# Performance work log

Hardware: AMD Instinct MI355X
Metric: run time of the kernel (lower is better)

The kernel has to match this reference:

```python
import jax, jax.numpy as jnp
import numpy as np

B, S, D, H, L, MAXSEQ = 32, 512, 768, 1024, 4, 1024


def setup_inputs() -> dict:
    key = jax.random.key(0)
    ks = jax.random.split(key, 10)
    s_in = 1.0 / np.sqrt(H)
    inp = {
        "x": jax.random.normal(ks[0], (B, S, D), dtype=jnp.float32),
        "pos_emb": jax.random.normal(ks[1], (1, MAXSEQ, D), dtype=jnp.float32),
        # layer 0 input->hidden weights (GRU: 3 gates stacked)
        "W_ih0": jax.random.uniform(ks[2], (3 * H, D), jnp.float32, -s_in, s_in),
        # layers 1..L-1 input->hidden weights
        "W_ih": jax.random.uniform(ks[3], (L - 1, 3 * H, H), jnp.float32, -s_in, s_in),
        "W_hh": jax.random.uniform(ks[4], (L, 3 * H, H), jnp.float32, -s_in, s_in),
        "b_ih": jax.random.uniform(ks[5], (L, 3 * H), jnp.float32, -s_in, s_in),
        "b_hh": jax.random.uniform(ks[6], (L, 3 * H), jnp.float32, -s_in, s_in),
        "W_out": jax.random.uniform(ks[7], (D, H), jnp.float32, -s_in, s_in),
        "b_out": jax.random.uniform(ks[8], (D,), jnp.float32, -s_in, s_in),
    }
    return inp


def _gru_cell(x, h, Wih, Whh, bih, bhh):
    # torch.nn.GRUCell math; gates stacked [r, z, n]
    gi = x @ Wih.T + bih  # [B, 3H]
    gh = h @ Whh.T + bhh  # [B, 3H]
    i_r, i_z, i_n = jnp.split(gi, 3, axis=-1)
    h_r, h_z, h_n = jnp.split(gh, 3, axis=-1)
    r = jax.nn.sigmoid(i_r + h_r)
    z = jax.nn.sigmoid(i_z + h_z)
    n = jnp.tanh(i_n + r * h_n)
    return (1.0 - z) * n + z * h


def reference(x, pos_emb, W_ih0, W_ih, W_hh, b_ih, b_hh, W_out, b_out):
    b, s, _ = x.shape
    xp = x + pos_emb[:, :s, :]          # add positional embedding
    xs = jnp.swapaxes(xp, 0, 1)         # [S, B, D] for scan over time

    def step(hs, xt):                   # hs: [L, B, H]
        inp = xt
        new_hs = []
        for l in range(L):
            Wih = W_ih0 if l == 0 else W_ih[l - 1]
            h = _gru_cell(inp, hs[l], Wih, W_hh[l], b_ih[l], b_hh[l])
            new_hs.append(h)
            inp = h
        return jnp.stack(new_hs), inp

    h0 = jnp.zeros((L, b, H), dtype=x.dtype)
    hs_final, outs = jax.lax.scan(step, h0, xs)  # outs: [S, B, H]
    out_seq = jnp.swapaxes(outs, 0, 1) @ W_out.T + b_out  # [B, S, D]
    return out_seq, hs_final
```

## Files before the change

### kernel.cpp

```cpp
#include <hip/hip_runtime.h>

#define B_ 32
#define S_ 512
#define D_ 768
#define H_ 1024
#define L_ 4
#define TH 3072
#define NPL 64
#define NITER (S_ + L_ - 1)

typedef unsigned short u16;
typedef unsigned int u32;
typedef __bf16 bf16x8 __attribute__((ext_vector_type(8)));
typedef float f32x4 __attribute__((ext_vector_type(4)));

__device__ __forceinline__ u16 f2b(float f) {
  unsigned u = __builtin_bit_cast(unsigned, f);
  u += 0x7fffu + ((u >> 16) & 1u);
  return (u16)(u >> 16);
}
__device__ __forceinline__ float b2f(u16 h) {
  return __builtin_bit_cast(float, ((unsigned)h) << 16);
}
__device__ __forceinline__ unsigned pack2(float a, float b) {
  return (unsigned)f2b(a) | ((unsigned)f2b(b) << 16);
}

__global__ __launch_bounds__(256) void cvt_kernel(const float* __restrict__ src,
                                                  u16* __restrict__ dst, int n4) {
  int i = blockIdx.x * 256 + threadIdx.x;
  int stride = gridDim.x * 256;
  for (; i < n4; i += stride) {
    float4 f = ((const float4*)src)[i];
    uint2 o;
    o.x = pack2(f.x, f.y);
    o.y = pack2(f.z, f.w);
    ((uint2*)dst)[i] = o;
  }
}

__global__ __launch_bounds__(256) void gi0_gemm(const float* __restrict__ x,
                                                const float* __restrict__ pos,
                                                const u16* __restrict__ W0,
                                                const float* __restrict__ bih0,
                                                u16* __restrict__ GI0) {
  const int n0 = blockIdx.x * 64;
  const int m0 = blockIdx.y * 64;
  __shared__ u16 sA[64 * 72];
  __shared__ u16 sB[64 * 72];
  const int tid = threadIdx.x, lane = tid & 63, wid = tid >> 6;
  const int wm = wid >> 1, wn = wid & 1;
  const int fr = lane & 15, fk = (lane >> 4) * 8;
  f32x4 acc[2][2] = {};
  for (int k0 = 0; k0 < D_; k0 += 64) {
    for (int sl = tid; sl < 512; sl += 256) {
      int r = sl >> 3, c = sl & 7;
      int m = m0 + r, si = m >> 5, b = m & 31;
      const float* xp = x + (size_t)((b << 9) + si) * D_ + k0 + c * 8;
      const float* pp = pos + (size_t)si * D_ + k0 + c * 8;
      float4 x0 = *(const float4*)xp, x1 = *(const float4*)(xp + 4);
      float4 p0 = *(const float4*)pp, p1 = *(const float4*)(pp + 4);
      uint4 o;
      o.x = pack2(x0.x + p0.x, x0.y + p0.y);
      o.y = pack2(x0.z + p0.z, x0.w + p0.w);
      o.z = pack2(x1.x + p1.x, x1.y + p1.y);
      o.w = pack2(x1.z + p1.z, x1.w + p1.w);
      *(uint4*)&sA[r * 72 + c * 8] = o;
      *(uint4*)&sB[r * 72 + c * 8] =
          *(const uint4*)(W0 + (size_t)(n0 + r) * D_ + k0 + c * 8);
    }
    __syncthreads();
#pragma unroll
    for (int kk = 0; kk < 2; ++kk) {
      bf16x8 a0 = *(const bf16x8*)&sA[(wm * 32 + fr) * 72 + kk * 32 + fk];
      bf16x8 a1 = *(const bf16x8*)&sA[(wm * 32 + 16 + fr) * 72 + kk * 32 + fk];
      bf16x8 b0 = *(const bf16x8*)&sB[(wn * 32 + fr) * 72 + kk * 32 + fk];
      bf16x8 b1 = *(const bf16x8*)&sB[(wn * 32 + 16 + fr) * 72 + kk * 32 + fk];
      acc[0][0] = __builtin_amdgcn_mfma_f32_16x16x32_bf16(a0, b0, acc[0][0], 0, 0, 0);
      acc[0][1] = __builtin_amdgcn_mfma_f32_16x16x32_bf16(a0, b1, acc[0][1], 0, 0, 0);
      acc[1][0] = __builtin_amdgcn_mfma_f32_16x16x32_bf16(a1, b0, acc[1][0], 0, 0, 0);
      acc[1][1] = __builtin_amdgcn_mfma_f32_16x16x32_bf16(a1, b1, acc[1][1], 0, 0, 0);
    }
    __syncthreads();
  }
#pragma unroll
  for (int mi = 0; mi < 2; ++mi)
#pragma unroll
    for (int ni = 0; ni < 2; ++ni)
#pragma unroll
      for (int r = 0; r < 4; ++r) {
        int m = m0 + wm * 32 + mi * 16 + (lane >> 4) * 4 + r;
        int n = n0 + wn * 32 + ni * 16 + fr;
        GI0[(size_t)m * TH + n] = f2b(acc[mi][ni][r] + bih0[n]);
      }
}

__global__ __launch_bounds__(256) void out_gemm(const u16* __restrict__ H3,
                                                const u16* __restrict__ Wo,
                                                const float* __restrict__ bo,
                                                float* __restrict__ out) {
  const int n0 = blockIdx.x * 64;
  const int m0 = blockIdx.y * 64;
  __shared__ u16 sA[64 * 72];
  __shared__ u16 sB[64 * 72];
  const int tid = threadIdx.x, lane = tid & 63, wid = tid >> 6;
  const int wm = wid >> 1, wn = wid & 1;
  const int fr = lane & 15, fk = (lane >> 4) * 8;
  f32x4 acc[2][2] = {};
  for (int k0 = 0; k0 < H_; k0 += 64) {
    for (int sl = tid; sl < 512; sl += 256) {
      int r = sl >> 3, c = sl & 7;
      int m = m0 + r, b = m >> 9, si = m & 511;
      *(uint4*)&sA[r * 72 + c * 8] =
          *(const uint4*)(H3 + (size_t)((si << 5) + b) * H_ + k0 + c * 8);
      *(uint4*)&sB[r * 72 + c * 8] =
          *(const uint4*)(Wo + (size_t)(n0 + r) * H_ + k0 + c * 8);
    }
    __syncthreads();
#pragma unroll
    for (int kk = 0; kk < 2; ++kk) {
      bf16x8 a0 = *(const bf16x8*)&sA[(wm * 32 + fr) * 72 + kk * 32 + fk];
      bf16x8 a1 = *(const bf16x8*)&sA[(wm * 32 + 16 + fr) * 72 + kk * 32 + fk];
      bf16x8 b0 = *(const bf16x8*)&sB[(wn * 32 + fr) * 72 + kk * 32 + fk];
      bf16x8 b1 = *(const bf16x8*)&sB[(wn * 32 + 16 + fr) * 72 + kk * 32 + fk];
      acc[0][0] = __builtin_amdgcn_mfma_f32_16x16x32_bf16(a0, b0, acc[0][0], 0, 0, 0);
      acc[0][1] = __builtin_amdgcn_mfma_f32_16x16x32_bf16(a0, b1, acc[0][1], 0, 0, 0);
      acc[1][0] = __builtin_amdgcn_mfma_f32_16x16x32_bf16(a1, b0, acc[1][0], 0, 0, 0);
      acc[1][1] = __builtin_amdgcn_mfma_f32_16x16x32_bf16(a1, b1, acc[1][1], 0, 0, 0);
    }
    __syncthreads();
  }
#pragma unroll
  for (int mi = 0; mi < 2; ++mi)
#pragma unroll
    for (int ni = 0; ni < 2; ++ni)
#pragma unroll
      for (int r = 0; r < 4; ++r) {
        int m = m0 + wm * 32 + mi * 16 + (lane >> 4) * 4 + r;
        int n = n0 + wn * 32 + ni * 16 + fr;
        out[(size_t)m * D_ + n] = acc[mi][ni][r] + bo[n];
      }
}

__global__ __launch_bounds__(256, 1) void rnn_persist(
    const u16* __restrict__ Whh, const u16* __restrict__ Wih,
    const u16* __restrict__ GI0, const float* __restrict__ bih,
    const float* __restrict__ bhh, u16* __restrict__ hg ,
    int* flags , u16* __restrict__ H3, float* __restrict__ hsf) {
  const int bid = blockIdx.x;
  const int l = bid >> 6;
  const int n0 = (bid & 63) << 4;
  const int tid = threadIdx.x, lane = tid & 63, wid = tid >> 6;
  const int fr = lane & 15, q = lane >> 4;

  __shared__ float red[4][3][32][17];

  bf16x8 w[3][16];
  if (l == 0) {
    const int kb = wid << 8;
#pragma unroll
    for (int g = 0; g < 3; ++g)
#pragma unroll
      for (int kt = 0; kt < 8; ++kt)
        w[g][kt] = *(const bf16x8*)(Whh + (((size_t)((g << 10) + n0 + fr)) << 10) +
                                    kb + kt * 32 + q * 8);
  } else {
    const u16* Wp = (wid < 2) ? (Wih + (((size_t)(l - 1) * TH) << 10))
                              : (Whh + (((size_t)l * TH) << 10));
    const int kb = (wid & 1) << 9;
#pragma unroll
    for (int g = 0; g < 3; ++g)
#pragma unroll
      for (int kt = 0; kt < 16; ++kt)
        w[g][kt] = *(const bf16x8*)(Wp + (((size_t)((g << 10) + n0 + fr)) << 10) +
                                    kb + kt * 32 + q * 8);
  }

  const int* f_own = flags + ((l << 6) + lane) * 16;
  const int* f_m1 = (l > 0) ? flags + (((l - 1) << 6) + lane) * 16 : f_own;
  const int* f_p1 = (l < 3) ? flags + (((l + 1) << 6) + lane) * 16 : f_own;
  int* f_mine = flags + ((l << 6) + (bid & 63)) * 16;

  const int gb = tid >> 3;
  const int gjj = (tid & 7) * 2;
  const int gj = n0 + gjj;
  float bihv[3][2], bhhv[3][2];
#pragma unroll
  for (int g = 0; g < 3; ++g) {
    if (l > 0) {
      bihv[g][0] = bih[l * TH + (g << 10) + gj];
      bihv[g][1] = bih[l * TH + (g << 10) + gj + 1];
    } else {
      bihv[g][0] = bihv[g][1] = 0.f;
    }
    bhhv[g][0] = bhh[l * TH + (g << 10) + gj];
    bhhv[g][1] = bhh[l * TH + (g << 10) + gj + 1];
  }
  float hpriv0 = 0.f, hpriv1 = 0.f;
  __syncthreads();

  for (int s = 0; s < NITER; ++s) {
    const int t = s - l;
    if (t < 0 || t >= S_) {
      if (tid == 0) {
        int v = s + 1;
        asm volatile("global_store_dword %0, %1, off sc0 sc1" ::"v"(f_mine), "v"(v)
                     : "memory");
      }
      continue;
    }
    const int prev = (s - 1) & 3;

    u32 g0p = 0, g1p = 0, g2p = 0;
    if (l == 0) {
      const u16* gp = GI0 + (size_t)((t << 5) + gb) * TH + gj;
      g0p = *(const u32*)gp;
      g1p = *(const u32*)(gp + 1024);
      g2p = *(const u32*)(gp + 2048);
    }

    if (wid == 0) {
      for (;;) {
        int fo, fm, fp;
        asm volatile(
            "global_load_dword %0, %3, off sc0 sc1\n\t"
            "global_load_dword %1, %4, off sc0 sc1\n\t"
            "global_load_dword %2, %5, off sc0 sc1\n\t"
            "s_waitcnt vmcnt(0)"
            : "=&v"(fo), "=&v"(fm), "=&v"(fp)
            : "v"(f_own), "v"(f_m1), "v"(f_p1)
            : "memory");
        __builtin_amdgcn_sched_barrier(0);
        bool ok = (fo >= s) && (fm >= s) && (fp >= s - 2);
        if (__all(ok)) break;
        __builtin_amdgcn_s_sleep(1);
      }
    }
    __syncthreads();

    f32x4 acc[2][3] = {};
    if (l == 0) {
      const u16* hp = hg + ((0 | prev) << 15);
      const int kb = wid << 8;
      bf16x8 afr[2][8];
#pragma unroll
      for (int mt = 0; mt < 2; ++mt)
#pragma unroll
        for (int kt = 0; kt < 8; ++kt) {
          const u16* p = hp + (((mt << 4) + fr) << 10) + kb + kt * 32 + q * 8;
          asm volatile("global_load_dwordx4 %0, %1, off sc0 sc1"
                       : "=v"(afr[mt][kt]) : "v"(p) : "memory");
        }
      asm volatile("s_waitcnt vmcnt(0)" ::: "memory");
      __builtin_amdgcn_sched_barrier(0);
#pragma unroll
      for (int kt = 0; kt < 8; ++kt)
#pragma unroll
        for (int g = 0; g < 3; ++g) {
          acc[0][g] = __builtin_amdgcn_mfma_f32_16x16x32_bf16(afr[0][kt], w[g][kt], acc[0][g], 0, 0, 0);
          acc[1][g] = __builtin_amdgcn_mfma_f32_16x16x32_bf16(afr[1][kt], w[g][kt], acc[1][g], 0, 0, 0);
        }
    } else {
      const u16* hsrc = (wid < 2) ? (hg + ((((l - 1) << 2) | prev) << 15))
                                  : (hg + (((l << 2) | prev) << 15));
      const int kb = (wid & 1) << 9;
      bf16x8 afr[2][16];
#pragma unroll
      for (int mt = 0; mt < 2; ++mt)
#pragma unroll
        for (int kt = 0; kt < 16; ++kt) {
          const u16* p = hsrc + (((mt << 4) + fr) << 10) + kb + kt * 32 + q * 8;
          asm volatile("global_load_dwordx4 %0, %1, off sc0 sc1"
                       : "=v"(afr[mt][kt]) : "v"(p) : "memory");
        }
      asm volatile("s_waitcnt vmcnt(0)" ::: "memory");
      __builtin_amdgcn_sched_barrier(0);
#pragma unroll
      for (int kt = 0; kt < 16; ++kt)
#pragma unroll
        for (int g = 0; g < 3; ++g) {
          acc[0][g] = __builtin_amdgcn_mfma_f32_16x16x32_bf16(afr[0][kt], w[g][kt], acc[0][g], 0, 0, 0);
          acc[1][g] = __builtin_amdgcn_mfma_f32_16x16x32_bf16(afr[1][kt], w[g][kt], acc[1][g], 0, 0, 0);
        }
    }

#pragma unroll
    for (int mt = 0; mt < 2; ++mt)
#pragma unroll
      for (int g = 0; g < 3; ++g)
#pragma unroll
        for (int r = 0; r < 4; ++r)
          red[wid][g][(mt << 4) + q * 4 + r][fr] = acc[mt][g][r];
    __syncthreads();

    float gi[3][2], gh[3][2];
#pragma unroll
    for (int g = 0; g < 3; ++g)
#pragma unroll
      for (int u = 0; u < 2; ++u) {
        float s01 = red[0][g][gb][gjj + u] + red[1][g][gb][gjj + u];
        float s23 = red[2][g][gb][gjj + u] + red[3][g][gb][gjj + u];
        if (l == 0) {
          gh[g][u] = s01 + s23 + bhhv[g][u];
        } else {
          gi[g][u] = s01 + bihv[g][u];
          gh[g][u] = s23 + bhhv[g][u];
        }
      }
    if (l == 0) {
      gi[0][0] = b2f((u16)(g0p & 0xffff));
      gi[0][1] = b2f((u16)(g0p >> 16));
      gi[1][0] = b2f((u16)(g1p & 0xffff));
      gi[1][1] = b2f((u16)(g1p >> 16));
      gi[2][0] = b2f((u16)(g2p & 0xffff));
      gi[2][1] = b2f((u16)(g2p >> 16));
    }
    float hn[2];
    float hpv[2] = {hpriv0, hpriv1};
#pragma unroll
    for (int u = 0; u < 2; ++u) {
      float rr = 1.f / (1.f + __expf(-(gi[0][u] + gh[0][u])));
      float zz = 1.f / (1.f + __expf(-(gi[1][u] + gh[1][u])));
      float xn = gi[2][u] + rr * gh[2][u];
      float nn = 1.f - 2.f / (__expf(2.f * xn) + 1.f);
      hn[u] = (1.f - zz) * nn + zz * hpv[u];
    }
    hpriv0 = hn[0];
    hpriv1 = hn[1];
    u32 hpack = pack2(hn[0], hn[1]);
    u32* hd = (u32*)(hg + (((l << 2) | (s & 3)) << 15) + (gb << 10) + gj);
    asm volatile("global_store_dword %0, %1, off sc0 sc1" ::"v"(hd), "v"(hpack)
                 : "memory");
    asm volatile("s_waitcnt vmcnt(0)" ::: "memory");
    __syncthreads();
    if (tid == 0) {
      int v = s + 1;
      asm volatile("global_store_dword %0, %1, off sc0 sc1" ::"v"(f_mine), "v"(v)
                   : "memory");
    }
    if (l == 3) *(u32*)(H3 + (((size_t)(t << 5) + gb) << 10) + gj) = hpack;
    if (t == S_ - 1) {
      hsf[((l << 5) + gb) * 1024 + gj] = hn[0];
      hsf[((l << 5) + gb) * 1024 + gj + 1] = hn[1];
    }
  }
}

extern "C" void kernel_launch(void* const* d_in, const int* in_sizes, int n_in,
                              void* d_out, int out_size, void* d_ws, size_t ws_size,
                              hipStream_t stream) {
  const float* x = (const float*)d_in[0];
  const float* pos = (const float*)d_in[1];
  const float* Wih0 = (const float*)d_in[2];
  const float* Wih = (const float*)d_in[3];
  const float* Whh = (const float*)d_in[4];
  const float* bih = (const float*)d_in[5];
  const float* bhh = (const float*)d_in[6];
  const float* Wout = (const float*)d_in[7];
  const float* bout = (const float*)d_in[8];
  float* out = (float*)d_out;

  char* ws = (char*)d_ws;
  size_t o = 0;
  u16* wih0_b = (u16*)(ws + o); o += (size_t)TH * D_ * 2;
  u16* wih_b  = (u16*)(ws + o); o += (size_t)3 * TH * H_ * 2;
  u16* whh_b  = (u16*)(ws + o); o += (size_t)4 * TH * H_ * 2;
  u16* wout_b = (u16*)(ws + o); o += (size_t)D_ * H_ * 2;
  u16* GI0    = (u16*)(ws + o); o += (size_t)S_ * B_ * TH * 2;
  u16* H3     = (u16*)(ws + o); o += (size_t)S_ * B_ * H_ * 2;
  u16* hg     = (u16*)(ws + o); o += (size_t)L_ * 4 * B_ * H_ * 2;
  int* flags  = (int*)(ws + o); o += (size_t)L_ * 64 * 16 * 4;

  cvt_kernel<<<512, 256, 0, stream>>>(Wih0, wih0_b, TH * D_ / 4);
  cvt_kernel<<<512, 256, 0, stream>>>(Wih, wih_b, 3 * TH * H_ / 4);
  cvt_kernel<<<512, 256, 0, stream>>>(Whh, whh_b, 4 * TH * H_ / 4);
  cvt_kernel<<<512, 256, 0, stream>>>(Wout, wout_b, D_ * H_ / 4);
  hipMemsetAsync(hg, 0, (size_t)L_ * 4 * B_ * H_ * 2 + (size_t)L_ * 64 * 16 * 4, stream);

  gi0_gemm<<<dim3(TH / 64, (S_ * B_) / 64), 256, 0, stream>>>(x, pos, wih0_b, bih, GI0);

  float* hsf = out + (size_t)B_ * S_ * D_;
  rnn_persist<<<256, 256, 0, stream>>>(whh_b, wih_b, GI0, bih, bhh, hg, flags, H3, hsf);

  out_gemm<<<dim3(D_ / 64, (S_ * B_) / 64), 256, 0, stream>>>(H3, wout_b, bout, out);
}
```

Before: 3.809 ms.

## Use 128 larger persistent blocks staging hidden state in LDS via direct loads

The persistent GRU kernel now runs 128 blocks of 512 threads instead of 256 blocks of 256 threads, with each block owning 32 output columns. Each step copies the previous hidden state(s) into LDS once per block with global_load_lds, and the waves read their MFMA A fragments from LDS rather than each wave loading them from global memory. The point is to cut duplicated global traffic for the hidden state and the number of blocks the flag barrier has to synchronise. In exchange each block needs about 129 KB of dynamic LDS, adds extra __syncthreads per step, and reads the biases from global memory inside the loop.

```diff
diff --git a/kernel.cpp b/kernel.cpp
--- a/kernel.cpp
+++ b/kernel.cpp
@@ -6,8 +6,10 @@
 #define H_ 1024
 #define L_ 4
 #define TH 3072
-#define NPL 64
+#define NPL 32
 #define NITER (S_ + L_ - 1)
+#define LDS_BUF 66048
+#define LDS_TOTAL 132096
 
 typedef unsigned short u16;
 typedef unsigned int u32;
@@ -142,60 +144,52 @@
       }
 }
 
-__global__ __launch_bounds__(256, 1) void rnn_persist(
+__global__ __launch_bounds__(512, 2) void rnn_persist(
     const u16* __restrict__ Whh, const u16* __restrict__ Wih,
     const u16* __restrict__ GI0, const float* __restrict__ bih,
     const float* __restrict__ bhh, u16* __restrict__ hg ,
     int* flags , u16* __restrict__ H3, float* __restrict__ hsf) {
+  extern __shared__ char smem[];
   const int bid = blockIdx.x;
-  const int l = bid >> 6;
-  const int n0 = (bid & 63) << 4;
+  const int l = bid >> 5;
+  const int n0 = (bid & 31) << 5;
   const int tid = threadIdx.x, lane = tid & 63, wid = tid >> 6;
   const int fr = lane & 15, q = lane >> 4;
-
-  __shared__ float red[4][3][32][17];
+  const int l32 = lane & 31;
+  const int nh = wid & 1;
 
   bf16x8 w[3][16];
   if (l == 0) {
-    const int kb = wid << 8;
+    const int kb = (wid >> 1) << 8;
 #pragma unroll
     for (int g = 0; g < 3; ++g)
 #pragma unroll
       for (int kt = 0; kt < 8; ++kt)
-        w[g][kt] = *(const bf16x8*)(Whh + (((size_t)((g << 10) + n0 + fr)) << 10) +
-                                    kb + kt * 32 + q * 8);
+        w[g][kt] = *(const bf16x8*)(
+            Whh + (((size_t)((g << 10) + n0 + nh * 16 + fr)) << 10) + kb +
+            kt * 32 + q * 8);
   } else {
-    const u16* Wp = (wid < 2) ? (Wih + (((size_t)(l - 1) * TH) << 10))
-                              : (Whh + (((size_t)l * TH) << 10));
-    const int kb = (wid & 1) << 9;
+    const int mat = wid >> 2;
+    const u16* Wp = (mat == 0) ? (Wih + (((size_t)(l - 1) * TH) << 10))
+                               : (Whh + (((size_t)l * TH) << 10));
+    const int kb = ((wid >> 1) & 1) << 9;
 #pragma unroll
     for (int g = 0; g < 3; ++g)
 #pragma unroll
       for (int kt = 0; kt < 16; ++kt)
-        w[g][kt] = *(const bf16x8*)(Wp + (((size_t)((g << 10) + n0 + fr)) << 10) +
-                                    kb + kt * 32 + q * 8);
+        w[g][kt] = *(const bf16x8*)(
+            Wp + (((size_t)((g << 10) + n0 + nh * 16 + fr)) << 10) + kb +
+            kt * 32 + q * 8);
   }
 
-  const int* f_own = flags + ((l << 6) + lane) * 16;
-  const int* f_m1 = (l > 0) ? flags + (((l - 1) << 6) + lane) * 16 : f_own;
-  const int* f_p1 = (l < 3) ? flags + (((l + 1) << 6) + lane) * 16 : f_own;
-  int* f_mine = flags + ((l << 6) + (bid & 63)) * 16;
-
-  const int gb = tid >> 3;
-  const int gjj = (tid & 7) * 2;
-  const int gj = n0 + gjj;
-  float bihv[3][2], bhhv[3][2];
-#pragma unroll
-  for (int g = 0; g < 3; ++g) {
-    if (l > 0) {
-      bihv[g][0] = bih[l * TH + (g << 10) + gj];
-      bihv[g][1] = bih[l * TH + (g << 10) + gj + 1];
-    } else {
-      bihv[g][0] = bihv[g][1] = 0.f;
-    }
-    bhhv[g][0] = bhh[l * TH + (g << 10) + gj];
-    bhhv[g][1] = bhh[l * TH + (g << 10) + gj + 1];
-  }
+  const int* f_own = flags + ((l << 5) + l32) * 16;
+  const int* f_m1 = (l > 0) ? flags + (((l - 1) << 5) + l32) * 16 : f_own;
+  const int* f_p1 = (l < 3) ? flags + (((l + 1) << 5) + l32) * 16 : f_own;
+  int* f_mine = flags + ((l << 5) + (bid & 31)) * 16;
+
+  const int gb = tid >> 4;
+  const int jj = (tid & 15) * 2;
+  const int gj = n0 + jj;
   float hpriv0 = 0.f, hpriv1 = 0.f;
   __syncthreads();
 
@@ -238,75 +232,104 @@
     }
     __syncthreads();
 
+    {
+      const u16* srcA = (l == 0) ? (hg + (prev << 15))
+                                 : (hg + ((((l - 1) << 2) | prev) << 15));
+      if (l == 0) {
+#pragma unroll
+        for (int ii = 0; ii < 8; ++ii) {
+          int i = wid * 8 + ii;
+          int row = i >> 1, half = i & 1;
+          const u16* sp = srcA + (row << 10) + half * 512 + lane * 8;
+          char* dp = smem + row * 2064 + half * 1024;
+          __builtin_amdgcn_global_load_lds(
+              (const __attribute__((address_space(1))) void*)sp,
+              (__attribute__((address_space(3))) void*)dp, 16, 0, 17);
+        }
+      } else {
+        const u16* srcB = hg + (((l << 2) | prev) << 15);
+#pragma unroll
+        for (int ii = 0; ii < 16; ++ii) {
+          int i = wid * 16 + ii;
+          int buf = i >> 6, j = i & 63, row = j >> 1, half = j & 1;
+          const u16* sp =
+              (buf ? srcB : srcA) + (row << 10) + half * 512 + lane * 8;
+          char* dp = smem + buf * LDS_BUF + row * 2064 + half * 1024;
+          __builtin_amdgcn_global_load_lds(
+              (const __attribute__((address_space(1))) void*)sp,
+              (__attribute__((address_space(3))) void*)dp, 16, 0, 17);
+        }
+      }
+      asm volatile("s_waitcnt vmcnt(0)" ::: "memory");
+    }
+    __syncthreads();
+
     f32x4 acc[2][3] = {};
     if (l == 0) {
-      const u16* hp = hg + ((0 | prev) << 15);
-      const int kb = wid << 8;
-      bf16x8 afr[2][8];
+      const int kqb = (wid >> 1) << 9;
+      const char* base = smem;
+#pragma unroll
+      for (int kt = 0; kt < 8; ++kt) {
+        int colb = kqb + kt * 64 + q * 16;
+        bf16x8 a0 = *(const bf16x8*)(base + fr * 2064 + colb);
+        bf16x8 a1 = *(const bf16x8*)(base + (16 + fr) * 2064 + colb);
+#pragma unroll
+        for (int g = 0; g < 3; ++g) {
+          acc[0][g] = __builtin_amdgcn_mfma_f32_16x16x32_bf16(a0, w[g][kt], acc[0][g], 0, 0, 0);
+          acc[1][g] = __builtin_amdgcn_mfma_f32_16x16x32_bf16(a1, w[g][kt], acc[1][g], 0, 0, 0);
+        }
+      }
+    } else {
+      const int khb = (((wid >> 1) & 1)) << 10;
+      const char* base = smem + (wid >> 2) * LDS_BUF;
+#pragma unroll
+      for (int kt = 0; kt < 16; ++kt) {
+        int colb = khb + kt * 64 + q * 16;
+        bf16x8 a0 = *(const bf16x8*)(base + fr * 2064 + colb);
+        bf16x8 a1 = *(const bf16x8*)(base + (16 + fr) * 2064 + colb);
+#pragma unroll
+        for (int g = 0; g < 3; ++g) {
+          acc[0][g] = __builtin_amdgcn_mfma_f32_16x16x32_bf16(a0, w[g][kt], acc[0][g], 0, 0, 0);
+          acc[1][g] = __builtin_amdgcn_mfma_f32_16x16x32_bf16(a1, w[g][kt], acc[1][g], 0, 0, 0);
+        }
+      }
+    }
+    __syncthreads();
+
+    {
+      float* red = (float*)smem;
+      const int slot = wid >> 1;
 #pragma unroll
       for (int mt = 0; mt < 2; ++mt)
 #pragma unroll
-        for (int kt = 0; kt < 8; ++kt) {
-          const u16* p = hp + (((mt << 4) + fr) << 10) + kb + kt * 32 + q * 8;
-          asm volatile("global_load_dwordx4 %0, %1, off sc0 sc1"
-                       : "=v"(afr[mt][kt]) : "v"(p) : "memory");
+        for (int g = 0; g < 3; ++g)
+#pragma unroll
+          for (int r = 0; r < 4; ++r)
+            red[((slot * 3 + g) * 32 + mt * 16 + q * 4 + r) * 33 + nh * 16 + fr] =
+                acc[mt][g][r];
+    }
+    __syncthreads();
+
+    float gi[3][2], gh[3][2];
+    {
+      const float* red = (const float*)smem;
+#pragma unroll
+      for (int g = 0; g < 3; ++g)
+#pragma unroll
+        for (int u = 0; u < 2; ++u) {
+          float s0 = red[((0 + g) * 32 + gb) * 33 + jj + u];
+          float s1 = red[((3 + g) * 32 + gb) * 33 + jj + u];
+          float s2 = red[((6 + g) * 32 + gb) * 33 + jj + u];
+          float s3 = red[((9 + g) * 32 + gb) * 33 + jj + u];
+          float bh = bhh[l * TH + (g << 10) + gj + u];
+          if (l == 0) {
+            gh[g][u] = s0 + s1 + s2 + s3 + bh;
+          } else {
+            gi[g][u] = s0 + s1 + bih[l * TH + (g << 10) + gj + u];
+            gh[g][u] = s2 + s3 + bh;
+          }
         }
-      asm volatile("s_waitcnt vmcnt(0)" ::: "memory");
-      __builtin_amdgcn_sched_barrier(0);
-#pragma unroll
-      for (int kt = 0; kt < 8; ++kt)
-#pragma unroll
-        for (int g = 0; g < 3; ++g) {
-          acc[0][g] = __builtin_amdgcn_mfma_f32_16x16x32_bf16(afr[0][kt], w[g][kt], acc[0][g], 0, 0, 0);
-          acc[1][g] = __builtin_amdgcn_mfma_f32_16x16x32_bf16(afr[1][kt], w[g][kt], acc[1][g], 0, 0, 0);
-        }
-    } else {
-      const u16* hsrc = (wid < 2) ? (hg + ((((l - 1) << 2) | prev) << 15))
-                                  : (hg + (((l << 2) | prev) << 15));
-      const int kb = (wid & 1) << 9;
-      bf16x8 afr[2][16];
-#pragma unroll
-      for (int mt = 0; mt < 2; ++mt)
-#pragma unroll
-        for (int kt = 0; kt < 16; ++kt) {
-          const u16* p = hsrc + (((mt << 4) + fr) << 10) + kb + kt * 32 + q * 8;
-          asm volatile("global_load_dwordx4 %0, %1, off sc0 sc1"
-                       : "=v"(afr[mt][kt]) : "v"(p) : "memory");
-        }
-      asm volatile("s_waitcnt vmcnt(0)" ::: "memory");
-      __builtin_amdgcn_sched_barrier(0);
-#pragma unroll
-      for (int kt = 0; kt < 16; ++kt)
-#pragma unroll
-        for (int g = 0; g < 3; ++g) {
-          acc[0][g] = __builtin_amdgcn_mfma_f32_16x16x32_bf16(afr[0][kt], w[g][kt], acc[0][g], 0, 0, 0);
-          acc[1][g] = __builtin_amdgcn_mfma_f32_16x16x32_bf16(afr[1][kt], w[g][kt], acc[1][g], 0, 0, 0);
-        }
-    }
-
-#pragma unroll
-    for (int mt = 0; mt < 2; ++mt)
-#pragma unroll
-      for (int g = 0; g < 3; ++g)
-#pragma unroll
-        for (int r = 0; r < 4; ++r)
-          red[wid][g][(mt << 4) + q * 4 + r][fr] = acc[mt][g][r];
-    __syncthreads();
-
-    float gi[3][2], gh[3][2];
-#pragma unroll
-    for (int g = 0; g < 3; ++g)
-#pragma unroll
-      for (int u = 0; u < 2; ++u) {
-        float s01 = red[0][g][gb][gjj + u] + red[1][g][gb][gjj + u];
-        float s23 = red[2][g][gb][gjj + u] + red[3][g][gb][gjj + u];
-        if (l == 0) {
-          gh[g][u] = s01 + s23 + bhhv[g][u];
-        } else {
-          gi[g][u] = s01 + bihv[g][u];
-          gh[g][u] = s23 + bhhv[g][u];
-        }
-      }
+    }
     if (l == 0) {
       gi[0][0] = b2f((u16)(g0p & 0xffff));
       gi[0][1] = b2f((u16)(g0p >> 16));
@@ -369,18 +392,22 @@
   u16* GI0    = (u16*)(ws + o); o += (size_t)S_ * B_ * TH * 2;
   u16* H3     = (u16*)(ws + o); o += (size_t)S_ * B_ * H_ * 2;
   u16* hg     = (u16*)(ws + o); o += (size_t)L_ * 4 * B_ * H_ * 2;
-  int* flags  = (int*)(ws + o); o += (size_t)L_ * 64 * 16 * 4;
+  int* flags  = (int*)(ws + o); o += (size_t)L_ * 32 * 16 * 4;
 
   cvt_kernel<<<512, 256, 0, stream>>>(Wih0, wih0_b, TH * D_ / 4);
   cvt_kernel<<<512, 256, 0, stream>>>(Wih, wih_b, 3 * TH * H_ / 4);
   cvt_kernel<<<512, 256, 0, stream>>>(Whh, whh_b, 4 * TH * H_ / 4);
   cvt_kernel<<<512, 256, 0, stream>>>(Wout, wout_b, D_ * H_ / 4);
-  hipMemsetAsync(hg, 0, (size_t)L_ * 4 * B_ * H_ * 2 + (size_t)L_ * 64 * 16 * 4, stream);
+  hipMemsetAsync(hg, 0, (size_t)L_ * 4 * B_ * H_ * 2 + (size_t)L_ * 32 * 16 * 4,
+                 stream);
 
   gi0_gemm<<<dim3(TH / 64, (S_ * B_) / 64), 256, 0, stream>>>(x, pos, wih0_b, bih, GI0);
 
   float* hsf = out + (size_t)B_ * S_ * D_;
-  rnn_persist<<<256, 256, 0, stream>>>(whh_b, wih_b, GI0, bih, bhh, hg, flags, H3, hsf);
+  hipFuncSetAttribute((const void*)rnn_persist,
+                      hipFuncAttributeMaxDynamicSharedMemorySize, LDS_TOTAL);
+  rnn_persist<<<128, 512, LDS_TOTAL, stream>>>(whh_b, wih_b, GI0, bih, bhh, hg,
+                                               flags, H3, hsf);
 
   out_gemm<<<dim3(D_ / 64, (S_ * B_) / 64), 256, 0, stream>>>(H3, wout_b, bout, out);
 }
```

New measurement: 5.000 ms. 1.31x slower.

## Halve persistent RNN blocks and stream weights from memory each step

Applied to the files above, without the earlier changes.

The persistent GRU kernel drops from 64 to 32 blocks per layer, so each block now covers 32 hidden columns instead of 16. Weight fragments are no longer held in registers; each timestep reloads them from global memory (L2) through per-row pointers. Each thread now handles four hidden units with wider loads and stores, and fewer blocks take part in the flag-based cross-block sync. The trade is less spin-wait and sync overhead against re-reading every weight from cache on every timestep, which adds memory latency to the serial critical path.

```diff
diff --git a/kernel.cpp b/kernel.cpp
--- a/kernel.cpp
+++ b/kernel.cpp
@@ -6,13 +6,14 @@
 #define H_ 1024
 #define L_ 4
 #define TH 3072
-#define NPL 64
+#define NPL 32
 #define NITER (S_ + L_ - 1)
 
 typedef unsigned short u16;
 typedef unsigned int u32;
 typedef __bf16 bf16x8 __attribute__((ext_vector_type(8)));
 typedef float f32x4 __attribute__((ext_vector_type(4)));
+typedef unsigned int u32x2 __attribute__((ext_vector_type(2)));
 
 __device__ __forceinline__ u16 f2b(float f) {
   unsigned u = __builtin_bit_cast(unsigned, f);
@@ -148,22 +149,23 @@
     const float* __restrict__ bhh, u16* __restrict__ hg ,
     int* flags , u16* __restrict__ H3, float* __restrict__ hsf) {
   const int bid = blockIdx.x;
-  const int l = bid >> 6;
-  const int n0 = (bid & 63) << 4;
+  const int l = bid >> 5;
+  const int n0 = (bid & 31) << 5;
   const int tid = threadIdx.x, lane = tid & 63, wid = tid >> 6;
   const int fr = lane & 15, q = lane >> 4;
-
-  __shared__ float red[4][3][32][17];
-
-  bf16x8 w[3][16];
+  const int l32 = lane & 31;
+
+  __shared__ float red[4][3][32][33];
+
+  const u16* wrow[3][2];
   if (l == 0) {
     const int kb = wid << 8;
 #pragma unroll
     for (int g = 0; g < 3; ++g)
 #pragma unroll
-      for (int kt = 0; kt < 8; ++kt)
-        w[g][kt] = *(const bf16x8*)(Whh + (((size_t)((g << 10) + n0 + fr)) << 10) +
-                                    kb + kt * 32 + q * 8);
+      for (int nh = 0; nh < 2; ++nh)
+        wrow[g][nh] =
+            Whh + (((size_t)((g << 10) + n0 + nh * 16 + fr)) << 10) + kb;
   } else {
     const u16* Wp = (wid < 2) ? (Wih + (((size_t)(l - 1) * TH) << 10))
                               : (Whh + (((size_t)l * TH) << 10));
@@ -171,32 +173,28 @@
 #pragma unroll
     for (int g = 0; g < 3; ++g)
 #pragma unroll
-      for (int kt = 0; kt < 16; ++kt)
-        w[g][kt] = *(const bf16x8*)(Wp + (((size_t)((g << 10) + n0 + fr)) << 10) +
-                                    kb + kt * 32 + q * 8);
+      for (int nh = 0; nh < 2; ++nh)
+        wrow[g][nh] =
+            Wp + (((size_t)((g << 10) + n0 + nh * 16 + fr)) << 10) + kb;
   }
 
-  const int* f_own = flags + ((l << 6) + lane) * 16;
-  const int* f_m1 = (l > 0) ? flags + (((l - 1) << 6) + lane) * 16 : f_own;
-  const int* f_p1 = (l < 3) ? flags + (((l + 1) << 6) + lane) * 16 : f_own;
-  int* f_mine = flags + ((l << 6) + (bid & 63)) * 16;
+  const int* f_own = flags + ((l << 5) + l32) * 16;
+  const int* f_m1 = (l > 0) ? flags + (((l - 1) << 5) + l32) * 16 : f_own;
+  const int* f_p1 = (l < 3) ? flags + (((l + 1) << 5) + l32) * 16 : f_own;
+  int* f_mine = flags + ((l << 5) + (bid & 31)) * 16;
 
   const int gb = tid >> 3;
-  const int gjj = (tid & 7) * 2;
-  const int gj = n0 + gjj;
-  float bihv[3][2], bhhv[3][2];
-#pragma unroll
-  for (int g = 0; g < 3; ++g) {
-    if (l > 0) {
-      bihv[g][0] = bih[l * TH + (g << 10) + gj];
-      bihv[g][1] = bih[l * TH + (g << 10) + gj + 1];
-    } else {
-      bihv[g][0] = bihv[g][1] = 0.f;
-    }
-    bhhv[g][0] = bhh[l * TH + (g << 10) + gj];
-    bhhv[g][1] = bhh[l * TH + (g << 10) + gj + 1];
-  }
-  float hpriv0 = 0.f, hpriv1 = 0.f;
+  const int jj = (tid & 7) * 4;
+  const int gj = n0 + jj;
+  float bihv[3][4], bhhv[3][4];
+#pragma unroll
+  for (int g = 0; g < 3; ++g)
+#pragma unroll
+    for (int u = 0; u < 4; ++u) {
+      bihv[g][u] = (l > 0) ? bih[l * TH + (g << 10) + gj + u] : 0.f;
+      bhhv[g][u] = bhh[l * TH + (g << 10) + gj + u];
+    }
+  float hpriv[4] = {0.f, 0.f, 0.f, 0.f};
   __syncthreads();
 
   for (int s = 0; s < NITER; ++s) {
@@ -211,12 +209,12 @@
     }
     const int prev = (s - 1) & 3;
 
-    u32 g0p = 0, g1p = 0, g2p = 0;
+    u32x2 g0p = {0, 0}, g1p = {0, 0}, g2p = {0, 0};
     if (l == 0) {
       const u16* gp = GI0 + (size_t)((t << 5) + gb) * TH + gj;
-      g0p = *(const u32*)gp;
-      g1p = *(const u32*)(gp + 1024);
-      g2p = *(const u32*)(gp + 2048);
+      g0p = *(const u32x2*)gp;
+      g1p = *(const u32x2*)(gp + 1024);
+      g2p = *(const u32x2*)(gp + 2048);
     }
 
     if (wid == 0) {
@@ -238,9 +236,9 @@
     }
     __syncthreads();
 
-    f32x4 acc[2][3] = {};
+    f32x4 acc[2][2][3] = {};
     if (l == 0) {
-      const u16* hp = hg + ((0 | prev) << 15);
+      const u16* hp = hg + (prev << 15);
       const int kb = wid << 8;
       bf16x8 afr[2][8];
 #pragma unroll
@@ -256,10 +254,13 @@
 #pragma unroll
       for (int kt = 0; kt < 8; ++kt)
 #pragma unroll
-        for (int g = 0; g < 3; ++g) {
-          acc[0][g] = __builtin_amdgcn_mfma_f32_16x16x32_bf16(afr[0][kt], w[g][kt], acc[0][g], 0, 0, 0);
-          acc[1][g] = __builtin_amdgcn_mfma_f32_16x16x32_bf16(afr[1][kt], w[g][kt], acc[1][g], 0, 0, 0);
-        }
+        for (int g = 0; g < 3; ++g)
+#pragma unroll
+          for (int nh = 0; nh < 2; ++nh) {
+            bf16x8 b = *(const bf16x8*)(wrow[g][nh] + kt * 32 + q * 8);
+            acc[0][nh][g] = __builtin_amdgcn_mfma_f32_16x16x32_bf16(afr[0][kt], b, acc[0][nh][g], 0, 0, 0);
+            acc[1][nh][g] = __builtin_amdgcn_mfma_f32_16x16x32_bf16(afr[1][kt], b, acc[1][nh][g], 0, 0, 0);
+          }
     } else {
       const u16* hsrc = (wid < 2) ? (hg + ((((l - 1) << 2) | prev) << 15))
                                   : (hg + (((l << 2) | prev) << 15));
@@ -278,10 +279,13 @@
 #pragma unroll
       for (int kt = 0; kt < 16; ++kt)
 #pragma unroll
-        for (int g = 0; g < 3; ++g) {
-          acc[0][g] = __builtin_amdgcn_mfma_f32_16x16x32_bf16(afr[0][kt], w[g][kt], acc[0][g], 0, 0, 0);
-          acc[1][g] = __builtin_amdgcn_mfma_f32_16x16x32_bf16(afr[1][kt], w[g][kt], acc[1][g], 0, 0, 0);
-        }
+        for (int g = 0; g < 3; ++g)
+#pragma unroll
+          for (int nh = 0; nh < 2; ++nh) {
+            bf16x8 b = *(const bf16x8*)(wrow[g][nh] + kt * 32 + q * 8);
+            acc[0][nh][g] = __builtin_amdgcn_mfma_f32_16x16x32_bf16(afr[0][kt], b, acc[0][nh][g], 0, 0, 0);
+            acc[1][nh][g] = __builtin_amdgcn_mfma_f32_16x16x32_bf16(afr[1][kt], b, acc[1][nh][g], 0, 0, 0);
+          }
     }
 
 #pragma unroll
@@ -289,47 +293,57 @@
 #pragma unroll
       for (int g = 0; g < 3; ++g)
 #pragma unroll
-        for (int r = 0; r < 4; ++r)
-          red[wid][g][(mt << 4) + q * 4 + r][fr] = acc[mt][g][r];
-    __syncthreads();
-
-    float gi[3][2], gh[3][2];
+        for (int nh = 0; nh < 2; ++nh)
+#pragma unroll
+          for (int r = 0; r < 4; ++r)
+            red[wid][g][(mt << 4) + q * 4 + r][nh * 16 + fr] = acc[mt][nh][g][r];
+    __syncthreads();
+
+    float gi[3][4], gh[3][4];
 #pragma unroll
     for (int g = 0; g < 3; ++g)
 #pragma unroll
-      for (int u = 0; u < 2; ++u) {
-        float s01 = red[0][g][gb][gjj + u] + red[1][g][gb][gjj + u];
-        float s23 = red[2][g][gb][gjj + u] + red[3][g][gb][gjj + u];
+      for (int u = 0; u < 4; ++u) {
+        float s0 = red[0][g][gb][jj + u];
+        float s1 = red[1][g][gb][jj + u];
+        float s2 = red[2][g][gb][jj + u];
+        float s3 = red[3][g][gb][jj + u];
         if (l == 0) {
-          gh[g][u] = s01 + s23 + bhhv[g][u];
+          gh[g][u] = s0 + s1 + s2 + s3 + bhhv[g][u];
         } else {
-          gi[g][u] = s01 + bihv[g][u];
-          gh[g][u] = s23 + bhhv[g][u];
+          gi[g][u] = s0 + s1 + bihv[g][u];
+          gh[g][u] = s2 + s3 + bhhv[g][u];
         }
       }
     if (l == 0) {
-      gi[0][0] = b2f((u16)(g0p & 0xffff));
-      gi[0][1] = b2f((u16)(g0p >> 16));
-      gi[1][0] = b2f((u16)(g1p & 0xffff));
-      gi[1][1] = b2f((u16)(g1p >> 16));
-      gi[2][0] = b2f((u16)(g2p & 0xffff));
-      gi[2][1] = b2f((u16)(g2p >> 16));
-    }
-    float hn[2];
-    float hpv[2] = {hpriv0, hpriv1};
-#pragma unroll
-    for (int u = 0; u < 2; ++u) {
+      gi[0][0] = b2f((u16)(g0p[0] & 0xffff));
+      gi[0][1] = b2f((u16)(g0p[0] >> 16));
+      gi[0][2] = b2f((u16)(g0p[1] & 0xffff));
+      gi[0][3] = b2f((u16)(g0p[1] >> 16));
+      gi[1][0] = b2f((u16)(g1p[0] & 0xffff));
+      gi[1][1] = b2f((u16)(g1p[0] >> 16));
+      gi[1][2] = b2f((u16)(g1p[1] & 0xffff));
+      gi[1][3] = b2f((u16)(g1p[1] >> 16));
+      gi[2][0] = b2f((u16)(g2p[0] & 0xffff));
+      gi[2][1] = b2f((u16)(g2p[0] >> 16));
+      gi[2][2] = b2f((u16)(g2p[1] & 0xffff));
+      gi[2][3] = b2f((u16)(g2p[1] >> 16));
+    }
+    float hn[4];
+#pragma unroll
+    for (int u = 0; u < 4; ++u) {
       float rr = 1.f / (1.f + __expf(-(gi[0][u] + gh[0][u])));
       float zz = 1.f / (1.f + __expf(-(gi[1][u] + gh[1][u])));
       float xn = gi[2][u] + rr * gh[2][u];
       float nn = 1.f - 2.f / (__expf(2.f * xn) + 1.f);
-      hn[u] = (1.f - zz) * nn + zz * hpv[u];
-    }
-    hpriv0 = hn[0];
-    hpriv1 = hn[1];
-    u32 hpack = pack2(hn[0], hn[1]);
+      hn[u] = (1.f - zz) * nn + zz * hpriv[u];
+      hpriv[u] = hn[u];
+    }
+    u32x2 hpack;
+    hpack[0] = pack2(hn[0], hn[1]);
+    hpack[1] = pack2(hn[2], hn[3]);
     u32* hd = (u32*)(hg + (((l << 2) | (s & 3)) << 15) + (gb << 10) + gj);
-    asm volatile("global_store_dword %0, %1, off sc0 sc1" ::"v"(hd), "v"(hpack)
+    asm volatile("global_store_dwordx2 %0, %1, off sc0 sc1" ::"v"(hd), "v"(hpack)
                  : "memory");
     asm volatile("s_waitcnt vmcnt(0)" ::: "memory");
     __syncthreads();
@@ -338,10 +352,10 @@
       asm volatile("global_store_dword %0, %1, off sc0 sc1" ::"v"(f_mine), "v"(v)
                    : "memory");
     }
-    if (l == 3) *(u32*)(H3 + (((size_t)(t << 5) + gb) << 10) + gj) = hpack;
+    if (l == 3) *(u32x2*)(H3 + (((size_t)(t << 5) + gb) << 10) + gj) = hpack;
     if (t == S_ - 1) {
-      hsf[((l << 5) + gb) * 1024 + gj] = hn[0];
-      hsf[((l << 5) + gb) * 1024 + gj + 1] = hn[1];
+      float4 hf = {hn[0], hn[1], hn[2], hn[3]};
+      *(float4*)(hsf + ((l << 5) + gb) * 1024 + gj) = hf;
     }
   }
 }
@@ -369,18 +383,20 @@
   u16* GI0    = (u16*)(ws + o); o += (size_t)S_ * B_ * TH * 2;
   u16* H3     = (u16*)(ws + o); o += (size_t)S_ * B_ * H_ * 2;
   u16* hg     = (u16*)(ws + o); o += (size_t)L_ * 4 * B_ * H_ * 2;
-  int* flags  = (int*)(ws + o); o += (size_t)L_ * 64 * 16 * 4;
+  int* flags  = (int*)(ws + o); o += (size_t)L_ * 32 * 16 * 4;
 
   cvt_kernel<<<512, 256, 0, stream>>>(Wih0, wih0_b, TH * D_ / 4);
   cvt_kernel<<<512, 256, 0, stream>>>(Wih, wih_b, 3 * TH * H_ / 4);
   cvt_kernel<<<512, 256, 0, stream>>>(Whh, whh_b, 4 * TH * H_ / 4);
   cvt_kernel<<<512, 256, 0, stream>>>(Wout, wout_b, D_ * H_ / 4);
-  hipMemsetAsync(hg, 0, (size_t)L_ * 4 * B_ * H_ * 2 + (size_t)L_ * 64 * 16 * 4, stream);
+  hipMemsetAsync(hg, 0, (size_t)L_ * 4 * B_ * H_ * 2 + (size_t)L_ * 32 * 16 * 4,
+                 stream);
 
   gi0_gemm<<<dim3(TH / 64, (S_ * B_) / 64), 256, 0, stream>>>(x, pos, wih0_b, bih, GI0);
 
   float* hsf = out + (size_t)B_ * S_ * D_;
-  rnn_persist<<<256, 256, 0, stream>>>(whh_b, wih_b, GI0, bih, bhh, hg, flags, H3, hsf);
+  rnn_persist<<<128, 256, 0, stream>>>(whh_b, wih_b, GI0, bih, bhh, hg, flags, H3,
+                                       hsf);
 
   out_gemm<<<dim3(D_ / 64, (S_ * B_) / 64), 256, 0, stream>>>(H3, wout_b, bout, out);
 }
```

Result: slower. 11.60 ms (+204.6%).

## Double persistent RNN block to 512 threads and split flag waits per wave

Applied to the files above, without the earlier changes.

Raises the persistent GRU kernel from 4 to 8 waves per block, so each wave holds half the K-slice of weights and issues half the loads and MFMAs per step. The elementwise gate stage now handles one column per thread. The dependency polling is also restructured: every wave spins on just the flag it needs (previous layer or own layer). The anti-overrun check on the next layer moves after the MMA, done by one wave, so it is off the critical path. The cost is a larger LDS reduction (8 partials) and per-thread 16-bit stores instead of packed 32-bit stores.

```diff
diff --git a/kernel.cpp b/kernel.cpp
--- a/kernel.cpp
+++ b/kernel.cpp
@@ -142,7 +142,7 @@
       }
 }
 
-__global__ __launch_bounds__(256, 1) void rnn_persist(
+__global__ __launch_bounds__(512, 1) void rnn_persist(
     const u16* __restrict__ Whh, const u16* __restrict__ Wih,
     const u16* __restrict__ GI0, const float* __restrict__ bih,
     const float* __restrict__ bhh, u16* __restrict__ hg ,
@@ -153,25 +153,26 @@
   const int tid = threadIdx.x, lane = tid & 63, wid = tid >> 6;
   const int fr = lane & 15, q = lane >> 4;
 
-  __shared__ float red[4][3][32][17];
-
-  bf16x8 w[3][16];
+  __shared__ float red[8][3][32][17];
+
+  bf16x8 w[3][8];
   if (l == 0) {
-    const int kb = wid << 8;
+    const int kb = wid << 7;
 #pragma unroll
     for (int g = 0; g < 3; ++g)
 #pragma unroll
-      for (int kt = 0; kt < 8; ++kt)
+      for (int kt = 0; kt < 4; ++kt)
         w[g][kt] = *(const bf16x8*)(Whh + (((size_t)((g << 10) + n0 + fr)) << 10) +
                                     kb + kt * 32 + q * 8);
   } else {
-    const u16* Wp = (wid < 2) ? (Wih + (((size_t)(l - 1) * TH) << 10))
-                              : (Whh + (((size_t)l * TH) << 10));
-    const int kb = (wid & 1) << 9;
+    const int mat = wid >> 2;
+    const u16* Wp = (mat == 0) ? (Wih + (((size_t)(l - 1) * TH) << 10))
+                               : (Whh + (((size_t)l * TH) << 10));
+    const int kb = (wid & 3) << 8;
 #pragma unroll
     for (int g = 0; g < 3; ++g)
 #pragma unroll
-      for (int kt = 0; kt < 16; ++kt)
+      for (int kt = 0; kt < 8; ++kt)
         w[g][kt] = *(const bf16x8*)(Wp + (((size_t)((g << 10) + n0 + fr)) << 10) +
                                     kb + kt * 32 + q * 8);
   }
@@ -180,23 +181,18 @@
   const int* f_m1 = (l > 0) ? flags + (((l - 1) << 6) + lane) * 16 : f_own;
   const int* f_p1 = (l < 3) ? flags + (((l + 1) << 6) + lane) * 16 : f_own;
   int* f_mine = flags + ((l << 6) + (bid & 63)) * 16;
-
-  const int gb = tid >> 3;
-  const int gjj = (tid & 7) * 2;
-  const int gj = n0 + gjj;
-  float bihv[3][2], bhhv[3][2];
+  const int* pw = (l > 0 && wid < 4) ? f_m1 : f_own;
+
+  const int gb = tid >> 4;
+  const int jj = tid & 15;
+  const int gj = n0 + jj;
+  float bihv[3], bhhv[3];
 #pragma unroll
   for (int g = 0; g < 3; ++g) {
-    if (l > 0) {
-      bihv[g][0] = bih[l * TH + (g << 10) + gj];
-      bihv[g][1] = bih[l * TH + (g << 10) + gj + 1];
-    } else {
-      bihv[g][0] = bihv[g][1] = 0.f;
-    }
-    bhhv[g][0] = bhh[l * TH + (g << 10) + gj];
-    bhhv[g][1] = bhh[l * TH + (g << 10) + gj + 1];
-  }
-  float hpriv0 = 0.f, hpriv1 = 0.f;
+    bihv[g] = (l > 0) ? bih[l * TH + (g << 10) + gj] : 0.f;
+    bhhv[g] = bhh[l * TH + (g << 10) + gj];
+  }
+  float hpriv = 0.f;
   __syncthreads();
 
   for (int s = 0; s < NITER; ++s) {
@@ -211,42 +207,32 @@
     }
     const int prev = (s - 1) & 3;
 
-    u32 g0p = 0, g1p = 0, g2p = 0;
+    float gp0 = 0.f, gp1 = 0.f, gp2 = 0.f;
     if (l == 0) {
       const u16* gp = GI0 + (size_t)((t << 5) + gb) * TH + gj;
-      g0p = *(const u32*)gp;
-      g1p = *(const u32*)(gp + 1024);
-      g2p = *(const u32*)(gp + 2048);
-    }
-
-    if (wid == 0) {
-      for (;;) {
-        int fo, fm, fp;
-        asm volatile(
-            "global_load_dword %0, %3, off sc0 sc1\n\t"
-            "global_load_dword %1, %4, off sc0 sc1\n\t"
-            "global_load_dword %2, %5, off sc0 sc1\n\t"
-            "s_waitcnt vmcnt(0)"
-            : "=&v"(fo), "=&v"(fm), "=&v"(fp)
-            : "v"(f_own), "v"(f_m1), "v"(f_p1)
-            : "memory");
-        __builtin_amdgcn_sched_barrier(0);
-        bool ok = (fo >= s) && (fm >= s) && (fp >= s - 2);
-        if (__all(ok)) break;
-        __builtin_amdgcn_s_sleep(1);
-      }
-    }
-    __syncthreads();
+      gp0 = b2f(gp[0]);
+      gp1 = b2f(gp[1024]);
+      gp2 = b2f(gp[2048]);
+    }
+
+    for (;;) {
+      int fv;
+      asm volatile("global_load_dword %0, %1, off sc0 sc1\n\ts_waitcnt vmcnt(0)"
+                   : "=v"(fv) : "v"(pw) : "memory");
+      __builtin_amdgcn_sched_barrier(0);
+      if (__all(fv >= s)) break;
+      __builtin_amdgcn_s_sleep(1);
+    }
 
     f32x4 acc[2][3] = {};
     if (l == 0) {
-      const u16* hp = hg + ((0 | prev) << 15);
-      const int kb = wid << 8;
-      bf16x8 afr[2][8];
+      const u16* hp = hg + (prev << 15);
+      const int kb = wid << 7;
+      bf16x8 afr[2][4];
 #pragma unroll
       for (int mt = 0; mt < 2; ++mt)
 #pragma unroll
-        for (int kt = 0; kt < 8; ++kt) {
+        for (int kt = 0; kt < 4; ++kt) {
           const u16* p = hp + (((mt << 4) + fr) << 10) + kb + kt * 32 + q * 8;
           asm volatile("global_load_dwordx4 %0, %1, off sc0 sc1"
                        : "=v"(afr[mt][kt]) : "v"(p) : "memory");
@@ -254,21 +240,21 @@
       asm volatile("s_waitcnt vmcnt(0)" ::: "memory");
       __builtin_amdgcn_sched_barrier(0);
 #pragma unroll
-      for (int kt = 0; kt < 8; ++kt)
+      for (int kt = 0; kt < 4; ++kt)
 #pragma unroll
         for (int g = 0; g < 3; ++g) {
           acc[0][g] = __builtin_amdgcn_mfma_f32_16x16x32_bf16(afr[0][kt], w[g][kt], acc[0][g], 0, 0, 0);
           acc[1][g] = __builtin_amdgcn_mfma_f32_16x16x32_bf16(afr[1][kt], w[g][kt], acc[1][g], 0, 0, 0);
         }
     } else {
-      const u16* hsrc = (wid < 2) ? (hg + ((((l - 1) << 2) | prev) << 15))
+      const u16* hsrc = (wid < 4) ? (hg + ((((l - 1) << 2) | prev) << 15))
                                   : (hg + (((l << 2) | prev) << 15));
-      const int kb = (wid & 1) << 9;
-      bf16x8 afr[2][16];
+      const int kb = (wid & 3) << 8;
+      bf16x8 afr[2][8];
 #pragma unroll
       for (int mt = 0; mt < 2; ++mt)
 #pragma unroll
-        for (int kt = 0; kt < 16; ++kt) {
+        for (int kt = 0; kt < 8; ++kt) {
           const u16* p = hsrc + (((mt << 4) + fr) << 10) + kb + kt * 32 + q * 8;
           asm volatile("global_load_dwordx4 %0, %1, off sc0 sc1"
                        : "=v"(afr[mt][kt]) : "v"(p) : "memory");
@@ -276,7 +262,7 @@
       asm volatile("s_waitcnt vmcnt(0)" ::: "memory");
       __builtin_amdgcn_sched_barrier(0);
 #pragma unroll
-      for (int kt = 0; kt < 16; ++kt)
+      for (int kt = 0; kt < 8; ++kt)
 #pragma unroll
         for (int g = 0; g < 3; ++g) {
           acc[0][g] = __builtin_amdgcn_mfma_f32_16x16x32_bf16(afr[0][kt], w[g][kt], acc[0][g], 0, 0, 0);
@@ -291,46 +277,52 @@
 #pragma unroll
         for (int r = 0; r < 4; ++r)
           red[wid][g][(mt << 4) + q * 4 + r][fr] = acc[mt][g][r];
-    __syncthreads();
-
-    float gi[3][2], gh[3][2];
-#pragma unroll
-    for (int g = 0; g < 3; ++g)
-#pragma unroll
-      for (int u = 0; u < 2; ++u) {
-        float s01 = red[0][g][gb][gjj + u] + red[1][g][gb][gjj + u];
-        float s23 = red[2][g][gb][gjj + u] + red[3][g][gb][gjj + u];
-        if (l == 0) {
-          gh[g][u] = s01 + s23 + bhhv[g][u];
-        } else {
-          gi[g][u] = s01 + bihv[g][u];
-          gh[g][u] = s23 + bhhv[g][u];
-        }
-      }
+
+    if (wid == 7) {
+      const int thr = s - 2;
+      for (;;) {
+        int fv;
+        asm volatile("global_load_dword %0, %1, off sc0 sc1\n\ts_waitcnt vmcnt(0)"
+                     : "=v"(fv) : "v"(f_p1) : "memory");
+        __builtin_amdgcn_sched_barrier(0);
+        if (__all(fv >= thr)) break;
+        __builtin_amdgcn_s_sleep(1);
+      }
+    }
+    __syncthreads();
+
+    float gi[3], gh[3];
+#pragma unroll
+    for (int g = 0; g < 3; ++g) {
+      float s0 = red[0][g][gb][jj] + red[1][g][gb][jj];
+      float s1 = red[2][g][gb][jj] + red[3][g][gb][jj];
+      float s2 = red[4][g][gb][jj] + red[5][g][gb][jj];
+      float s3 = red[6][g][gb][jj] + red[7][g][gb][jj];
+      if (l == 0) {
+        gh[g] = s0 + s1 + s2 + s3 + bhhv[g];
+      } else {
+        gi[g] = s0 + s1 + bihv[g];
+        gh[g] = s2 + s3 + bhhv[g];
+      }
+    }
     if (l == 0) {
-      gi[0][0] = b2f((u16)(g0p & 0xffff));
-      gi[0][1] = b2f((u16)(g0p >> 16));
-      gi[1][0] = b2f((u16)(g1p & 0xffff));
-      gi[1][1] = b2f((u16)(g1p >> 16));
-      gi[2][0] = b2f((u16)(g2p & 0xffff));
-      gi[2][1] = b2f((u16)(g2p >> 16));
-    }
-    float hn[2];
-    float hpv[2] = {hpriv0, hpriv1};
-#pragma unroll
-    for (int u = 0; u < 2; ++u) {
-      float rr = 1.f / (1.f + __expf(-(gi[0][u] + gh[0][u])));
-      float zz = 1.f / (1.f + __expf(-(gi[1][u] + gh[1][u])));
-      float xn = gi[2][u] + rr * gh[2][u];
-      float nn = 1.f - 2.f / (__expf(2.f * xn) + 1.f);
-      hn[u] = (1.f - zz) * nn + zz * hpv[u];
-    }
-    hpriv0 = hn[0];
-    hpriv1 = hn[1];
-    u32 hpack = pack2(hn[0], hn[1]);
-    u32* hd = (u32*)(hg + (((l << 2) | (s & 3)) << 15) + (gb << 10) + gj);
-    asm volatile("global_store_dword %0, %1, off sc0 sc1" ::"v"(hd), "v"(hpack)
-                 : "memory");
+      gi[0] = gp0;
+      gi[1] = gp1;
+      gi[2] = gp2;
+    }
+    float rr = 1.f / (1.f + __expf(-(gi[0] + gh[0])));
+    float zz = 1.f / (1.f + __expf(-(gi[1] + gh[1])));
+    float xn = gi[2] + rr * gh[2];
+    float nn = 1.f - 2.f / (__expf(2.f * xn) + 1.f);
+    float hn = (1.f - zz) * nn + zz * hpriv;
+    hpriv = hn;
+    u16 hb = f2b(hn);
+    u16* hd = hg + (((l << 2) | (s & 3)) << 15) + (gb << 10) + gj;
+    {
+      u32 hv = hb;
+      asm volatile("global_store_short %0, %1, off sc0 sc1" ::"v"(hd), "v"(hv)
+                   : "memory");
+    }
     asm volatile("s_waitcnt vmcnt(0)" ::: "memory");
     __syncthreads();
     if (tid == 0) {
@@ -338,11 +330,8 @@
       asm volatile("global_store_dword %0, %1, off sc0 sc1" ::"v"(f_mine), "v"(v)
                    : "memory");
     }
-    if (l == 3) *(u32*)(H3 + (((size_t)(t << 5) + gb) << 10) + gj) = hpack;
-    if (t == S_ - 1) {
-      hsf[((l << 5) + gb) * 1024 + gj] = hn[0];
-      hsf[((l << 5) + gb) * 1024 + gj + 1] = hn[1];
-    }
+    if (l == 3) H3[(((size_t)(t << 5) + gb) << 10) + gj] = hb;
+    if (t == S_ - 1) hsf[((l << 5) + gb) * 1024 + gj] = hn;
   }
 }
 
@@ -375,12 +364,14 @@
   cvt_kernel<<<512, 256, 0, stream>>>(Wih, wih_b, 3 * TH * H_ / 4);
   cvt_kernel<<<512, 256, 0, stream>>>(Whh, whh_b, 4 * TH * H_ / 4);
   cvt_kernel<<<512, 256, 0, stream>>>(Wout, wout_b, D_ * H_ / 4);
-  hipMemsetAsync(hg, 0, (size_t)L_ * 4 * B_ * H_ * 2 + (size_t)L_ * 64 * 16 * 4, stream);
+  hipMemsetAsync(hg, 0, (size_t)L_ * 4 * B_ * H_ * 2 + (size_t)L_ * 64 * 16 * 4,
+                 stream);
 
   gi0_gemm<<<dim3(TH / 64, (S_ * B_) / 64), 256, 0, stream>>>(x, pos, wih0_b, bih, GI0);
 
   float* hsf = out + (size_t)B_ * S_ * D_;
-  rnn_persist<<<256, 256, 0, stream>>>(whh_b, wih_b, GI0, bih, bhh, hg, flags, H3, hsf);
+  rnn_persist<<<256, 512, 0, stream>>>(whh_b, wih_b, GI0, bih, bhh, hg, flags, H3,
+                                       hsf);
 
   out_gemm<<<dim3(D_ / 64, (S_ * B_) / 64), 256, 0, stream>>>(H3, wout_b, bout, out);
 }
```

Result: faster. 3.529 ms (-7.3%).
